# Performance work log

Hardware: AMD Instinct MI355X
Metric: run time of the kernel (lower is better)

The kernel has to match this reference:

```python
import jax, jax.numpy as jnp
import numpy as np

ROPE_THETA = 10000.0

def _apply_rope(x, theta=ROPE_THETA):
    # x: [B, H, L, d_head]
    L, d_k = x.shape[-2], x.shape[-1]
    inv_freq = 1.0 / (theta ** (jnp.arange(0, d_k, 2, dtype=jnp.float32) / d_k))  # [d_k/2]
    ang = jnp.arange(L, dtype=jnp.float32)[:, None] * inv_freq[None, :]           # [L, d_k/2]
    ang = jnp.repeat(ang, 2, axis=-1)                                             # [L, d_k] interleaved
    xr = x.reshape(x.shape[:-1] + (d_k // 2, 2))
    rot = jnp.stack((-xr[..., 1], xr[..., 0]), axis=-1).reshape(x.shape)
    return x * jnp.cos(ang) + rot * jnp.sin(ang)

def setup_inputs() -> dict:
    key = jax.random.key(0)
    k1, k2, k3 = jax.random.split(key, 3)
    B, L, D = 2, 2048, 2048
    std_qkv = np.sqrt(2.0 / (D + 3 * D)).astype(np.float32)
    std_o = np.sqrt(2.0 / (D + D)).astype(np.float32)
    return {
        "x": jax.random.normal(k1, (B, L, D), dtype=jnp.float32),
        "W_qkv": jax.random.normal(k2, (3 * D, D), dtype=jnp.float32) * std_qkv,
        "W_o": jax.random.normal(k3, (D, D), dtype=jnp.float32) * std_o,
    }

def reference(x, W_qkv, W_o):
    B, L, D = x.shape
    H = 16
    dh = D // H
    qkv = jnp.einsum('bld,ed->ble', x, W_qkv)            # [B, L, 3D]
    q, k, v = jnp.split(qkv, 3, axis=-1)
    # [B, H, L, dh]
    q = q.reshape(B, L, H, dh).transpose(0, 2, 1, 3)
    k = k.reshape(B, L, H, dh).transpose(0, 2, 1, 3)
    v = v.reshape(B, L, H, dh).transpose(0, 2, 1, 3)
    q = _apply_rope(q)
    k = _apply_rope(k)
    scale = 1.0 / np.sqrt(dh).astype(np.float32)
    att = jnp.einsum('bhqd,bhkd->bhqk', q, k) * scale    # [B, H, L, L]
    causal = jnp.tril(jnp.ones((L, L), dtype=bool))
    att = jnp.where(causal, att, -jnp.inf)
    p = jax.nn.softmax(att, axis=-1)
    y = jnp.einsum('bhqk,bhkd->bhqd', p, v)              # [B, H, L, dh]
    y = y.transpose(0, 2, 1, 3).reshape(B, L, D)
    return jnp.einsum('bld,ed->ble', y, W_o)
```

## Files before the change

kernel.cpp:

```cpp
#include <hip/hip_runtime.h>
#include <math.h>

typedef __bf16 bf16x8 __attribute__((ext_vector_type(8)));
typedef float f32x4 __attribute__((ext_vector_type(4)));
typedef unsigned short us8 __attribute__((ext_vector_type(8)));

#define B_ 2
#define L_ 2048
#define D_ 2048
#define H_ 16
#define DH 128

__device__ __forceinline__ unsigned short f2b(float f) {
  union { float f; unsigned u; } v; v.f = f;
  unsigned u = v.u;
  return (unsigned short)((u + 0x7fffu + ((u >> 16) & 1u)) >> 16);
}
__device__ __forceinline__ float b2f(unsigned short h) {
  union { unsigned u; float f; } v; v.u = ((unsigned)h) << 16;
  return v.f;
}

#define GLD16(g, l) __builtin_amdgcn_global_load_lds(                          \
    (const __attribute__((address_space(1))) void*)(g),                        \
    (__attribute__((address_space(3))) void*)(l), 16, 0, 0)

#define SBAR() __builtin_amdgcn_s_barrier()
#define LGK0() asm volatile("s_waitcnt lgkmcnt(0)")
#define SCB0() __builtin_amdgcn_sched_barrier(0)
#define VMC6() asm volatile("s_waitcnt vmcnt(6)" ::: "memory")
#define VMC3() asm volatile("s_waitcnt vmcnt(3)" ::: "memory")
#define VMC0() asm volatile("s_waitcnt vmcnt(0)" ::: "memory")

__device__ __forceinline__ unsigned ldsoff(const void* p) {
  return (unsigned)(unsigned long long)(const __attribute__((address_space(3))) char*)p;
}
__device__ __forceinline__ bf16x8 dsr128(unsigned a) {
  bf16x8 r;
  asm volatile("ds_read_b128 %0, %1" : "=v"(r) : "v"(a));
  return r;
}

__global__ void f32_to_bf16_3(const float* __restrict__ a, int na4,
                              const float* __restrict__ b, int nb4,
                              const float* __restrict__ c, int nc4,
                              unsigned short* __restrict__ oa,
                              unsigned short* __restrict__ ob,
                              unsigned short* __restrict__ oc) {
  const int total = na4 + nb4 + nc4;
  int i = blockIdx.x * blockDim.x + threadIdx.x;
  const int stride = gridDim.x * blockDim.x;
  for (; i < total; i += stride) {
    const float* src;
    unsigned short* dst;
    int j = i;
    if (j < na4) { src = a; dst = oa; }
    else if (j < na4 + nb4) { j -= na4; src = b; dst = ob; }
    else { j -= na4 + nb4; src = c; dst = oc; }
    const float4 v = ((const float4*)src)[j];
    ushort4 o;
    o.x = f2b(v.x); o.y = f2b(v.y); o.z = f2b(v.z); o.w = f2b(v.w);
    ((ushort4*)dst)[j] = o;
  }
}

template <bool OUT_BF16>
__global__ __launch_bounds__(256, 2)
void gemmw128(const unsigned short* __restrict__ A,
              const unsigned short* __restrict__ Bm,
              void* __restrict__ Cv, int M, int N, int K) {
  __shared__ __align__(16) unsigned short lA[3][128 * 32];
  __shared__ __align__(16) unsigned short lB[3][256 * 32];
  const int tid = threadIdx.x;
  const int w = tid >> 6, lane = tid & 63;
  const int lo = lane & 15, hi = lane >> 4;
  const int mh = w >> 1;
  const int nh = w & 1;
  const int GM = M >> 7;
  const int nwg = gridDim.x;
  const int f = blockIdx.x;
  const int v = (f & 7) * (nwg >> 3) + (f >> 3);
  const int bn = v / GM, bm = v % GM;
  const int NT = K >> 5;

  const int srow = tid >> 2;
  const int gs = (tid & 3) ^ ((srow >> 1) & 3);
  auto stA = [&](int buf, int u, int tile) {
    GLD16(A + (long)(bm * 128 + u * 64 + srow) * K + tile * 32 + gs * 8,
          &lA[buf][u * 2048 + tid * 8]);
  };
  auto stB = [&](int buf, int u, int tile) {
    GLD16(Bm + (long)(bn * 256 + u * 64 + srow) * K + tile * 32 + gs * 8,
          &lB[buf][u * 2048 + tid * 8]);
  };

  unsigned aoff[4], boff[8];
#pragma unroll
  for (int mi = 0; mi < 4; ++mi) {
    const int r = mh * 64 + mi * 16 + lo;
    aoff[mi] = ldsoff(&lA[0][0]) + r * 64 + ((hi ^ ((r >> 1) & 3)) * 16);
  }
#pragma unroll
  for (int ni = 0; ni < 8; ++ni) {
    const int rb = nh * 128 + ni * 16 + lo;
    boff[ni] = ldsoff(&lB[0][0]) + rb * 64 + ((hi ^ ((rb >> 1) & 3)) * 16);
  }

  f32x4 acc[4][8] = {};

  stA(0, 0, 0); stA(0, 1, 0);
  stB(0, 0, 0); stB(0, 1, 0); stB(0, 2, 0); stB(0, 3, 0);
  stA(1, 0, 1); stA(1, 1, 1);
  stB(1, 0, 1); stB(1, 1, 1); stB(1, 2, 1); stB(1, 3, 1);
  VMC6();
  SBAR();

  for (int t = 0; t < NT; ++t) {
    const int bt = t % 3;
    const int b2 = (t + 2) % 3;
    const bool nx = (t + 2 < NT);
    const unsigned ab = (unsigned)(bt * 8192);
    const unsigned bb = (unsigned)(bt * 16384);
    bf16x8 af[4], bfv[8];
#pragma unroll
    for (int mi = 0; mi < 4; ++mi) af[mi] = dsr128(aoff[mi] + ab);
#pragma unroll
    for (int ni = 0; ni < 8; ++ni) bfv[ni] = dsr128(boff[ni] + bb);
    if (nx) {
      stA(b2, 0, t + 2); stA(b2, 1, t + 2);
      stB(b2, 0, t + 2); stB(b2, 1, t + 2);
      stB(b2, 2, t + 2); stB(b2, 3, t + 2);
    }
    LGK0(); SCB0();
    __builtin_amdgcn_s_setprio(1);
#pragma unroll
    for (int ni = 0; ni < 8; ++ni)
#pragma unroll
      for (int mi = 0; mi < 4; ++mi)
        acc[mi][ni] = __builtin_amdgcn_mfma_f32_16x16x32_bf16(
            af[mi], bfv[ni], acc[mi][ni], 0, 0, 0);
    __builtin_amdgcn_s_setprio(0);
    if (t < NT - 2) VMC6(); else VMC0();
    SBAR();
  }

  const int r0 = bm * 128 + mh * 64;
  const int c0 = bn * 256 + nh * 128;
#pragma unroll
  for (int mi = 0; mi < 4; ++mi) {
#pragma unroll
    for (int r = 0; r < 4; ++r) {
      const long row = r0 + mi * 16 + hi * 4 + r;
#pragma unroll
      for (int ni = 0; ni < 8; ++ni) {
        const int col = c0 + ni * 16 + lo;
        if (OUT_BF16)
          ((unsigned short*)Cv)[row * N + col] = f2b(acc[mi][ni][r]);
        else
          ((float*)Cv)[row * N + col] = acc[mi][ni][r];
      }
    }
  }
}

template <bool OUT_BF16>
__global__ __launch_bounds__(512, 4)
void gemmk32(const unsigned short* __restrict__ A,
             const unsigned short* __restrict__ Bm,
             void* __restrict__ Cv, int M, int N, int K) {
  __shared__ __align__(16) unsigned short lA[3][128 * 32];
  __shared__ __align__(16) unsigned short lB[3][256 * 32];
  const int tid = threadIdx.x;
  const int w = tid >> 6, lane = tid & 63;
  const int lo = lane & 15, hi = lane >> 4;
  const int mh = w >> 2;
  const int wn = (w & 3) * 64;
  const int GM = M >> 7;
  const int nwg = gridDim.x;
  const int f = blockIdx.x;
  const int v = (f & 7) * (nwg >> 3) + (f >> 3);
  const int bn = v / GM, bm = v % GM;
  const int NT = K >> 5;

  const int srow = tid >> 2;
  const int gs = (tid & 3) ^ ((srow >> 1) & 3);
  auto stA = [&](int buf, int tile) {
    GLD16(A + (long)(bm * 128 + srow) * K + tile * 32 + gs * 8,
          &lA[buf][(tid & ~63) * 8]);
  };
  auto stB = [&](int buf, int u, int tile) {
    GLD16(Bm + (long)(bn * 256 + u * 128 + srow) * K + tile * 32 + gs * 8,
          &lB[buf][u * 4096 + (tid & ~63) * 8]);
  };

  unsigned aoff[4], boff[4];
#pragma unroll
  for (int mi = 0; mi < 4; ++mi) {
    const int r = mh * 64 + mi * 16 + lo;
    aoff[mi] = ldsoff(&lA[0][0]) + r * 64 + ((hi ^ ((r >> 1) & 3)) * 16);
  }
#pragma unroll
  for (int ni = 0; ni < 4; ++ni) {
    const int rb = wn + ni * 16 + lo;
    boff[ni] = ldsoff(&lB[0][0]) + rb * 64 + ((hi ^ ((rb >> 1) & 3)) * 16);
  }

  f32x4 acc[4][4] = {};

  stA(0, 0); stB(0, 0, 0); stB(0, 1, 0);
  stA(1, 1); stB(1, 0, 1); stB(1, 1, 1);
  VMC3();
  SBAR();

  for (int t = 0; t < NT; ++t) {
    const int bt = t % 3;
    const int b2 = (t + 2) % 3;
    const bool nx = (t + 2 < NT);
    const unsigned ab = (unsigned)(bt * 8192);
    const unsigned bb = (unsigned)(bt * 16384);
    bf16x8 af[4], bfv[4];
#pragma unroll
    for (int mi = 0; mi < 4; ++mi) af[mi] = dsr128(aoff[mi] + ab);
#pragma unroll
    for (int ni = 0; ni < 4; ++ni) bfv[ni] = dsr128(boff[ni] + bb);
    if (nx) { stA(b2, t + 2); stB(b2, 0, t + 2); stB(b2, 1, t + 2); }
    LGK0(); SCB0();
    __builtin_amdgcn_s_setprio(1);
#pragma unroll
    for (int mi = 0; mi < 4; ++mi)
#pragma unroll
      for (int ni = 0; ni < 4; ++ni)
        acc[mi][ni] = __builtin_amdgcn_mfma_f32_16x16x32_bf16(
            af[mi], bfv[ni], acc[mi][ni], 0, 0, 0);
    __builtin_amdgcn_s_setprio(0);
    if (t < NT - 2) VMC3(); else VMC0();
    SBAR();
  }

  const int r0 = bm * 128 + mh * 64;
  const int c0 = bn * 256 + wn;
#pragma unroll
  for (int mi = 0; mi < 4; ++mi) {
#pragma unroll
    for (int r = 0; r < 4; ++r) {
      const long row = r0 + mi * 16 + hi * 4 + r;
#pragma unroll
      for (int ni = 0; ni < 4; ++ni) {
        const int col = c0 + ni * 16 + lo;
        if (OUT_BF16)
          ((unsigned short*)Cv)[row * N + col] = f2b(acc[mi][ni][r]);
        else
          ((float*)Cv)[row * N + col] = acc[mi][ni][r];
      }
    }
  }
}

__global__ void rope_qk(const unsigned short* __restrict__ qkv,
                        unsigned short* __restrict__ Qo,
                        unsigned short* __restrict__ Ko) {
  const int idx = blockIdx.x * 256 + threadIdx.x;
  const int i = idx & 63;
  const int l = (idx >> 6) & (L_ - 1);
  const int h = (idx >> 17) & (H_ - 1);
  const int b = idx >> 21;
  const float invf = exp2f(-(float)i * 0.20762050593045077f);
  const float ang = (float)l * invf;
  float sn, cs;
  sincosf(ang, &sn, &cs);
  const long base = ((long)b * L_ + l) * (3 * D_) + h * DH + 2 * i;
  const unsigned qin = *(const unsigned*)&qkv[base];
  const unsigned kin = *(const unsigned*)&qkv[base + D_];
  const float q0 = b2f((unsigned short)qin), q1 = b2f((unsigned short)(qin >> 16));
  const float k0 = b2f((unsigned short)kin), k1 = b2f((unsigned short)(kin >> 16));
  const float sc = 0.12751743f;
  const float qo0 = (q0 * cs - q1 * sn) * sc, qo1 = (q1 * cs + q0 * sn) * sc;
  const float ko0 = (k0 * cs - k1 * sn), ko1 = (k1 * cs + k0 * sn);
  const long oo = ((long)(b * H_ + h) * L_ + l) * DH + 2 * i;
  *(unsigned*)&Qo[oo] = (unsigned)f2b(qo0) | ((unsigned)f2b(qo1) << 16);
  *(unsigned*)&Ko[oo] = (unsigned)f2b(ko0) | ((unsigned)f2b(ko1) << 16);
}

__global__ __launch_bounds__(256)
void v_fragpack(const unsigned short* __restrict__ qkv,
                unsigned short* __restrict__ Vf) {
  const int lblk = blockIdx.x;
  const int bh = blockIdx.y;
  const int b = bh >> 4, h = bh & 15;
  __shared__ unsigned short tile[64 * 137];
  const int tid = threadIdx.x;
  const int l0 = lblk * 64;
#pragma unroll
  for (int j = 0; j < 4; ++j) {
    const int c = j * 256 + tid;
    const int row = c >> 4, col8 = c & 15;
    const us8 v = *(const us8*)&qkv[((long)b * L_ + l0 + row) * (3 * D_) +
                                    2 * D_ + h * DH + col8 * 8];
    unsigned short* dst = &tile[row * 137 + col8 * 8];
#pragma unroll
    for (int e = 0; e < 8; ++e) dst[e] = v[e];
  }
  __syncthreads();
#pragma unroll
  for (int j = 0; j < 4; ++j) {
    const int c = j * 256 + tid;
    const int k32l = c >> 9, t2 = (c >> 6) & 7, lane = c & 63;
    const int lo = lane & 15, hi = lane >> 4;
    us8 v;
#pragma unroll
    for (int e = 0; e < 8; ++e)
      v[e] = tile[(k32l * 32 + hi * 8 + e) * 137 + t2 * 16 + lo];
    *(us8*)&Vf[(((size_t)bh * 64 + lblk * 2 + k32l) * 8 + t2) * 512 + lane * 8] = v;
  }
}

__global__ __launch_bounds__(256, 2)
void flash_attn3(const unsigned short* __restrict__ Q,
                 const unsigned short* __restrict__ Kg,
                 const unsigned short* __restrict__ Vf,
                 unsigned short* __restrict__ Y) {
  const int p = blockIdx.x;
  const int tA = p, tB = (L_ / 64 - 1) - p;
  const int h = blockIdx.y, b = blockIdx.z;
  const int tid = threadIdx.x;
  const int wave = tid >> 6, lane = tid & 63;
  const int lo = lane & 15, hi = lane >> 4;
  const int swz = (lo & 7) << 4;
  const int qA = tA * 64 + wave * 16;
  const int qB = tB * 64 + wave * 16;
  const long hoff = ((long)(b * H_ + h)) * L_ * DH;
  const unsigned short* Qh = Q + hoff;
  const unsigned short* Kh = Kg + hoff;
  const unsigned short* Vfh = Vf + ((size_t)(b * H_ + h)) * (64 * 8 * 512);

  __shared__ unsigned short lK[2][64 * 128];
  __shared__ unsigned short pl[4][2][16 * 72];
  unsigned short* plA = &pl[wave][0][0];
  unsigned short* plB = &pl[wave][1][0];

  auto stage = [&](int bufi, int kv0s) {
    unsigned short* bk = &lK[bufi][0];
#pragma unroll
    for (int j = 0; j < 4; ++j) {
      const int c = j * 256 + tid;
      const int row = c >> 4;
      const int soff = ((c & 15) ^ (row & 7)) << 3;
      GLD16(Kh + (long)(kv0s + row) * DH + soff, &bk[(c & ~63) * 8]);
    }
  };

  bf16x8 qfA[4], qfB[4];
#pragma unroll
  for (int s = 0; s < 4; ++s) {
    qfA[s] = *(const bf16x8*)&Qh[(long)(qA + lo) * DH + s * 32 + hi * 8];
    qfB[s] = *(const bf16x8*)&Qh[(long)(qB + lo) * DH + s * 32 + hi * 8];
  }

  float mA = -INFINITY, lsA = 0.f, mB = -INFINITY, lsB = 0.f;
  f32x4 yA[8] = {}, yB[8] = {};

  auto softmax = [&](f32x4 (&st)[4], float& m, float& lsum, f32x4 (&yacc)[8],
                     unsigned short* plw, int qw, int kv0) {
    if (kv0 + 63 > qw) {
      const int d0 = qw + lo - kv0 - hi * 4;
#pragma unroll
      for (int t = 0; t < 4; ++t) {
        const int dt = d0 - t * 16;
#pragma unroll
        for (int r = 0; r < 4; ++r)
          if (r > dt) st[t][r] = -INFINITY;
      }
    }
    float tm0 = fmaxf(fmaxf(st[0][0], st[0][1]), fmaxf(st[0][2], st[0][3]));
    float tm1 = fmaxf(fmaxf(st[1][0], st[1][1]), fmaxf(st[1][2], st[1][3]));
    float tm2 = fmaxf(fmaxf(st[2][0], st[2][1]), fmaxf(st[2][2], st[2][3]));
    float tm3 = fmaxf(fmaxf(st[3][0], st[3][1]), fmaxf(st[3][2], st[3][3]));
    float rm = fmaxf(fmaxf(tm0, tm1), fmaxf(tm2, tm3));
    rm = fmaxf(rm, __shfl_xor(rm, 16));
    rm = fmaxf(rm, __shfl_xor(rm, 32));
    if (!__all(rm <= m + 8.f)) {
      const float mn = fmaxf(m, rm);
      const float alpha = exp2f(m - mn);
      m = mn;
      lsum *= alpha;
      float ar[4];
#pragma unroll
      for (int r = 0; r < 4; ++r) ar[r] = __shfl(alpha, hi * 4 + r);
#pragma unroll
      for (int t2 = 0; t2 < 8; ++t2)
#pragma unroll
        for (int r = 0; r < 4; ++r) yacc[t2][r] *= ar[r];
    }
    float rs = 0.f;
#pragma unroll
    for (int t = 0; t < 4; ++t) {
#pragma unroll
      for (int r2 = 0; r2 < 2; ++r2) {
        const float e0 = exp2f(st[t][2 * r2] - m);
        const float e1 = exp2f(st[t][2 * r2 + 1] - m);
        rs += e0 + e1;
        const unsigned short u0 = __builtin_bit_cast(unsigned short, (__bf16)e0);
        const unsigned short u1 = __builtin_bit_cast(unsigned short, (__bf16)e1);
        *(unsigned*)&plw[lo * 72 + t * 16 + hi * 4 + 2 * r2] =
            (unsigned)u0 | ((unsigned)u1 << 16);
      }
    }
    rs += __shfl_xor(rs, 16);
    rs += __shfl_xor(rs, 32);
    lsum += rs;
  };

  const int nIter = tB + 1;
  stage(0, 0);
  __syncthreads();

  for (int it = 0; it < nIter; ++it) {
    const int kv0 = it * 64;
    const bool aAct = (it <= tA);
    if (it + 1 < nIter) stage((it + 1) & 1, kv0 + 64);
    const char* bkc = (const char*)&lK[it & 1][0];
    f32x4 stA[4] = {}, stB[4] = {};
    if (aAct) {
#pragma unroll
      for (int s = 0; s < 4; ++s) {
        const int inner = (lo * 256 + s * 64 + hi * 16) ^ swz;
#pragma unroll
        for (int t = 0; t < 4; ++t) {
          const bf16x8 kf = *(const bf16x8*)(bkc + t * 4096 + inner);
          stA[t] = __builtin_amdgcn_mfma_f32_16x16x32_bf16(kf, qfA[s], stA[t], 0, 0, 0);
          stB[t] = __builtin_amdgcn_mfma_f32_16x16x32_bf16(kf, qfB[s], stB[t], 0, 0, 0);
        }
      }
    } else {
#pragma unroll
      for (int s = 0; s < 4; ++s) {
        const int inner = (lo * 256 + s * 64 + hi * 16) ^ swz;
#pragma unroll
        for (int t = 0; t < 4; ++t) {
          const bf16x8 kf = *(const bf16x8*)(bkc + t * 4096 + inner);
          stB[t] = __builtin_amdgcn_mfma_f32_16x16x32_bf16(kf, qfB[s], stB[t], 0, 0, 0);
        }
      }
    }
    const unsigned short* vbase = Vfh + (size_t)(it * 16) * 512 + lane * 8;
    bf16x8 vf[16];
#pragma unroll
    for (int t2 = 0; t2 < 16; ++t2)
      vf[t2] = *(const bf16x8*)(vbase + (size_t)t2 * 512);
    if (aAct) softmax(stA, mA, lsA, yA, plA, qA, kv0);
    softmax(stB, mB, lsB, yB, plB, qB, kv0);
#pragma unroll
    for (int kt = 0; kt < 2; ++kt) {
      const bf16x8 pfB = *(const bf16x8*)&plB[lo * 72 + kt * 32 + hi * 8];
#pragma unroll
      for (int t2 = 0; t2 < 8; ++t2)
        yB[t2] = __builtin_amdgcn_mfma_f32_16x16x32_bf16(pfB, vf[kt * 8 + t2], yB[t2], 0, 0, 0);
      if (aAct) {
        const bf16x8 pfA = *(const bf16x8*)&plA[lo * 72 + kt * 32 + hi * 8];
#pragma unroll
        for (int t2 = 0; t2 < 8; ++t2)
          yA[t2] = __builtin_amdgcn_mfma_f32_16x16x32_bf16(pfA, vf[kt * 8 + t2], yA[t2], 0, 0, 0);
      }
    }
    __syncthreads();
  }

  auto wout = [&](f32x4 (&yacc)[8], float lsum, int qw) {
    const float inv = 1.f / lsum;
    float ir[4];
#pragma unroll
    for (int r = 0; r < 4; ++r) ir[r] = __shfl(inv, hi * 4 + r);
#pragma unroll
    for (int r = 0; r < 4; ++r) {
      const long row = qw + hi * 4 + r;
      unsigned short* yrow = Y + ((long)b * L_ + row) * D_ + h * DH;
#pragma unroll
      for (int t2 = 0; t2 < 8; ++t2)
        yrow[t2 * 16 + lo] = f2b(yacc[t2][r] * ir[r]);
    }
  };
  wout(yA, lsA, qA);
  wout(yB, lsB, qB);
}

extern "C" void kernel_launch(void* const* d_in, const int* in_sizes, int n_in,
                              void* d_out, int out_size, void* d_ws, size_t ws_size,
                              hipStream_t stream) {
  const float* x = (const float*)d_in[0];
  const float* wqkv = (const float*)d_in[1];
  const float* wo = (const float*)d_in[2];
  float* out = (float*)d_out;

  unsigned short* ws = (unsigned short*)d_ws;
  const size_t N_X = (size_t)B_ * L_ * D_;
  const size_t N_WQKV = (size_t)3 * D_ * D_;
  const size_t N_WO = (size_t)D_ * D_;
  const size_t N_QKV = (size_t)B_ * L_ * 3 * D_;
  const size_t N_HEAD = (size_t)B_ * H_ * L_ * DH;
  unsigned short* xb = ws;
  unsigned short* wqkb = xb + N_X;
  unsigned short* wob = wqkb + N_WQKV;
  unsigned short* qkv = wob + N_WO;
  unsigned short* Qb = qkv + N_QKV;
  unsigned short* Kb = Qb + N_HEAD;
  unsigned short* Vf = Kb + N_HEAD;
  unsigned short* Yb = Vf + N_HEAD;
  const size_t need = (size_t)(Yb + N_HEAD - ws) * sizeof(unsigned short);
  if (ws_size < need) return;

  f32_to_bf16_3<<<2048, 256, 0, stream>>>(
      x, (int)(N_X / 4), wqkv, (int)(N_WQKV / 4), wo, (int)(N_WO / 4),
      xb, wqkb, wob);

  gemmw128<true><<<(B_ * L_ / 128) * (3 * D_ / 256), 256, 0, stream>>>(
      xb, wqkb, qkv, B_ * L_, 3 * D_, D_);

  rope_qk<<<(B_ * H_ * L_ * 64) / 256, 256, 0, stream>>>(qkv, Qb, Kb);
  v_fragpack<<<dim3(L_ / 64, B_ * H_), 256, 0, stream>>>(qkv, Vf);

  flash_attn3<<<dim3(16, H_, B_), 256, 0, stream>>>(Qb, Kb, Vf, Yb);

  gemmk32<false><<<(B_ * L_ / 128) * (D_ / 256), 512, 0, stream>>>(
      Yb, wob, out, B_ * L_, D_, D_);
}
```

Measured before the change: 278.0 us.

## Fuse RoPE, Q scaling and V fragment packing into QKV GEMM epilogue

The QKV projection GEMM now runs with 512 threads in a 2x4 wave layout, as in the output GEMM. Its epilogue writes Q and K with RoPE and the Q scale applied, and writes V directly in the fragment-packed layout. This removes the separate rope_qk and v_fragpack kernels and the bf16 qkv intermediate round trip through global memory. The cost is heavier epilogue math (hardware sin/cos, shuffles) and scattered 2-byte stores for Q/K, plus the change in wave tiling.

```diff
diff --git a/kernel.cpp b/kernel.cpp
--- a/kernel.cpp
+++ b/kernel.cpp
@@ -28,7 +28,6 @@
 #define SBAR() __builtin_amdgcn_s_barrier()
 #define LGK0() asm volatile("s_waitcnt lgkmcnt(0)")
 #define SCB0() __builtin_amdgcn_sched_barrier(0)
-#define VMC6() asm volatile("s_waitcnt vmcnt(6)" ::: "memory")
 #define VMC3() asm volatile("s_waitcnt vmcnt(3)" ::: "memory")
 #define VMC0() asm volatile("s_waitcnt vmcnt(0)" ::: "memory")
 
@@ -64,18 +63,19 @@
   }
 }
 
-template <bool OUT_BF16>
-__global__ __launch_bounds__(256, 2)
-void gemmw128(const unsigned short* __restrict__ A,
+__global__ __launch_bounds__(512, 4)
+void gemm_qkv(const unsigned short* __restrict__ A,
               const unsigned short* __restrict__ Bm,
-              void* __restrict__ Cv, int M, int N, int K) {
+              unsigned short* __restrict__ Qb,
+              unsigned short* __restrict__ Kb,
+              unsigned short* __restrict__ Vf, int M, int K) {
   __shared__ __align__(16) unsigned short lA[3][128 * 32];
   __shared__ __align__(16) unsigned short lB[3][256 * 32];
   const int tid = threadIdx.x;
   const int w = tid >> 6, lane = tid & 63;
   const int lo = lane & 15, hi = lane >> 4;
-  const int mh = w >> 1;
-  const int nh = w & 1;
+  const int mh = w >> 2;
+  const int wn = (w & 3) * 64;
   const int GM = M >> 7;
   const int nwg = gridDim.x;
   const int f = blockIdx.x;
@@ -85,34 +85,32 @@
 
   const int srow = tid >> 2;
   const int gs = (tid & 3) ^ ((srow >> 1) & 3);
-  auto stA = [&](int buf, int u, int tile) {
-    GLD16(A + (long)(bm * 128 + u * 64 + srow) * K + tile * 32 + gs * 8,
-          &lA[buf][u * 2048 + tid * 8]);
+  auto stA = [&](int buf, int tile) {
+    GLD16(A + (long)(bm * 128 + srow) * K + tile * 32 + gs * 8,
+          &lA[buf][(tid & ~63) * 8]);
   };
   auto stB = [&](int buf, int u, int tile) {
-    GLD16(Bm + (long)(bn * 256 + u * 64 + srow) * K + tile * 32 + gs * 8,
-          &lB[buf][u * 2048 + tid * 8]);
-  };
-
-  unsigned aoff[4], boff[8];
+    GLD16(Bm + (long)(bn * 256 + u * 128 + srow) * K + tile * 32 + gs * 8,
+          &lB[buf][u * 4096 + (tid & ~63) * 8]);
+  };
+
+  unsigned aoff[4], boff[4];
 #pragma unroll
   for (int mi = 0; mi < 4; ++mi) {
     const int r = mh * 64 + mi * 16 + lo;
     aoff[mi] = ldsoff(&lA[0][0]) + r * 64 + ((hi ^ ((r >> 1) & 3)) * 16);
   }
 #pragma unroll
-  for (int ni = 0; ni < 8; ++ni) {
-    const int rb = nh * 128 + ni * 16 + lo;
+  for (int ni = 0; ni < 4; ++ni) {
+    const int rb = wn + ni * 16 + lo;
     boff[ni] = ldsoff(&lB[0][0]) + rb * 64 + ((hi ^ ((rb >> 1) & 3)) * 16);
   }
 
-  f32x4 acc[4][8] = {};
-
-  stA(0, 0, 0); stA(0, 1, 0);
-  stB(0, 0, 0); stB(0, 1, 0); stB(0, 2, 0); stB(0, 3, 0);
-  stA(1, 0, 1); stA(1, 1, 1);
-  stB(1, 0, 1); stB(1, 1, 1); stB(1, 2, 1); stB(1, 3, 1);
-  VMC6();
+  f32x4 acc[4][4] = {};
+
+  stA(0, 0); stB(0, 0, 0); stB(0, 1, 0);
+  stA(1, 1); stB(1, 0, 1); stB(1, 1, 1);
+  VMC3();
   SBAR();
 
   for (int t = 0; t < NT; ++t) {
@@ -121,43 +119,70 @@
     const bool nx = (t + 2 < NT);
     const unsigned ab = (unsigned)(bt * 8192);
     const unsigned bb = (unsigned)(bt * 16384);
-    bf16x8 af[4], bfv[8];
+    bf16x8 af[4], bfv[4];
 #pragma unroll
     for (int mi = 0; mi < 4; ++mi) af[mi] = dsr128(aoff[mi] + ab);
 #pragma unroll
-    for (int ni = 0; ni < 8; ++ni) bfv[ni] = dsr128(boff[ni] + bb);
-    if (nx) {
-      stA(b2, 0, t + 2); stA(b2, 1, t + 2);
-      stB(b2, 0, t + 2); stB(b2, 1, t + 2);
-      stB(b2, 2, t + 2); stB(b2, 3, t + 2);
-    }
+    for (int ni = 0; ni < 4; ++ni) bfv[ni] = dsr128(boff[ni] + bb);
+    if (nx) { stA(b2, t + 2); stB(b2, 0, t + 2); stB(b2, 1, t + 2); }
     LGK0(); SCB0();
     __builtin_amdgcn_s_setprio(1);
 #pragma unroll
-    for (int ni = 0; ni < 8; ++ni)
-#pragma unroll
-      for (int mi = 0; mi < 4; ++mi)
+    for (int mi = 0; mi < 4; ++mi)
+#pragma unroll
+      for (int ni = 0; ni < 4; ++ni)
         acc[mi][ni] = __builtin_amdgcn_mfma_f32_16x16x32_bf16(
             af[mi], bfv[ni], acc[mi][ni], 0, 0, 0);
     __builtin_amdgcn_s_setprio(0);
-    if (t < NT - 2) VMC6(); else VMC0();
+    if (t < NT - 2) VMC3(); else VMC0();
     SBAR();
   }
 
   const int r0 = bm * 128 + mh * 64;
-  const int c0 = bn * 256 + nh * 128;
-#pragma unroll
-  for (int mi = 0; mi < 4; ++mi) {
-#pragma unroll
-    for (int r = 0; r < 4; ++r) {
-      const long row = r0 + mi * 16 + hi * 4 + r;
-#pragma unroll
-      for (int ni = 0; ni < 8; ++ni) {
-        const int col = c0 + ni * 16 + lo;
-        if (OUT_BF16)
-          ((unsigned short*)Cv)[row * N + col] = f2b(acc[mi][ni][r]);
-        else
-          ((float*)Cv)[row * N + col] = acc[mi][ni][r];
+  const int h = (bn & 7) * 2 + (wn >> 7);
+  const int d0 = wn & 64;
+  if (bn < 16) {
+    unsigned short* dst = (bn < 8) ? Qb : Kb;
+    const float sc = (bn < 8) ? 0.12751743f : 1.0f;
+#pragma unroll
+    for (int ni = 0; ni < 4; ++ni) {
+      const int d = d0 + ni * 16 + lo;
+      const float invr = exp2f(-(float)(d >> 1) * 0.20762050593045077f) *
+                         0.15915494309189535f;
+#pragma unroll
+      for (int mi = 0; mi < 4; ++mi) {
+#pragma unroll
+        for (int r = 0; r < 4; ++r) {
+          const int row = r0 + mi * 16 + hi * 4 + r;
+          const int b = row >> 11, l = row & (L_ - 1);
+          const float rev = __builtin_amdgcn_fractf((float)l * invr);
+          const float sn = __builtin_amdgcn_sinf(rev);
+          const float cs = __builtin_amdgcn_cosf(rev);
+          const float v0 = acc[mi][ni][r] * sc;
+          const float vp = __shfl_xor(v0, 1);
+          const float ov = (d & 1) ? (v0 * cs + vp * sn)
+                                   : (v0 * cs - vp * sn);
+          dst[((long)(b * H_ + h) * L_ + l) * DH + d] = f2b(ov);
+        }
+      }
+    }
+  } else {
+#pragma unroll
+    for (int ni = 0; ni < 4; ++ni) {
+      const int d = d0 + ni * 16 + lo;
+#pragma unroll
+      for (int mi = 0; mi < 4; ++mi) {
+        const int row0 = r0 + mi * 16 + hi * 4;
+        const int b = row0 >> 11, l0 = row0 & (L_ - 1);
+        const size_t base =
+            (((size_t)(b * H_ + h) * 64 + (l0 >> 5)) * 8 + (d >> 4)) * 512;
+        const int fl = (d & 15) + ((l0 >> 3) & 3) * 16;
+        ushort4 pk;
+        pk.x = f2b(acc[mi][ni][0]);
+        pk.y = f2b(acc[mi][ni][1]);
+        pk.z = f2b(acc[mi][ni][2]);
+        pk.w = f2b(acc[mi][ni][3]);
+        *(ushort4*)&Vf[base + fl * 8 + (l0 & 7)] = pk;
       }
     }
   }
@@ -256,64 +281,6 @@
   }
 }
 
-__global__ void rope_qk(const unsigned short* __restrict__ qkv,
-                        unsigned short* __restrict__ Qo,
-                        unsigned short* __restrict__ Ko) {
-  const int idx = blockIdx.x * 256 + threadIdx.x;
-  const int i = idx & 63;
-  const int l = (idx >> 6) & (L_ - 1);
-  const int h = (idx >> 17) & (H_ - 1);
-  const int b = idx >> 21;
-  const float invf = exp2f(-(float)i * 0.20762050593045077f);
-  const float ang = (float)l * invf;
-  float sn, cs;
-  sincosf(ang, &sn, &cs);
-  const long base = ((long)b * L_ + l) * (3 * D_) + h * DH + 2 * i;
-  const unsigned qin = *(const unsigned*)&qkv[base];
-  const unsigned kin = *(const unsigned*)&qkv[base + D_];
-  const float q0 = b2f((unsigned short)qin), q1 = b2f((unsigned short)(qin >> 16));
-  const float k0 = b2f((unsigned short)kin), k1 = b2f((unsigned short)(kin >> 16));
-  const float sc = 0.12751743f;
-  const float qo0 = (q0 * cs - q1 * sn) * sc, qo1 = (q1 * cs + q0 * sn) * sc;
-  const float ko0 = (k0 * cs - k1 * sn), ko1 = (k1 * cs + k0 * sn);
-  const long oo = ((long)(b * H_ + h) * L_ + l) * DH + 2 * i;
-  *(unsigned*)&Qo[oo] = (unsigned)f2b(qo0) | ((unsigned)f2b(qo1) << 16);
-  *(unsigned*)&Ko[oo] = (unsigned)f2b(ko0) | ((unsigned)f2b(ko1) << 16);
-}
-
-__global__ __launch_bounds__(256)
-void v_fragpack(const unsigned short* __restrict__ qkv,
-                unsigned short* __restrict__ Vf) {
-  const int lblk = blockIdx.x;
-  const int bh = blockIdx.y;
-  const int b = bh >> 4, h = bh & 15;
-  __shared__ unsigned short tile[64 * 137];
-  const int tid = threadIdx.x;
-  const int l0 = lblk * 64;
-#pragma unroll
-  for (int j = 0; j < 4; ++j) {
-    const int c = j * 256 + tid;
-    const int row = c >> 4, col8 = c & 15;
-    const us8 v = *(const us8*)&qkv[((long)b * L_ + l0 + row) * (3 * D_) +
-                                    2 * D_ + h * DH + col8 * 8];
-    unsigned short* dst = &tile[row * 137 + col8 * 8];
-#pragma unroll
-    for (int e = 0; e < 8; ++e) dst[e] = v[e];
-  }
-  __syncthreads();
-#pragma unroll
-  for (int j = 0; j < 4; ++j) {
-    const int c = j * 256 + tid;
-    const int k32l = c >> 9, t2 = (c >> 6) & 7, lane = c & 63;
-    const int lo = lane & 15, hi = lane >> 4;
-    us8 v;
-#pragma unroll
-    for (int e = 0; e < 8; ++e)
-      v[e] = tile[(k32l * 32 + hi * 8 + e) * 137 + t2 * 16 + lo];
-    *(us8*)&Vf[(((size_t)bh * 64 + lblk * 2 + k32l) * 8 + t2) * 512 + lane * 8] = v;
-  }
-}
-
 __global__ __launch_bounds__(256, 2)
 void flash_attn3(const unsigned short* __restrict__ Q,
                  const unsigned short* __restrict__ Kg,
@@ -495,13 +462,11 @@
   const size_t N_X = (size_t)B_ * L_ * D_;
   const size_t N_WQKV = (size_t)3 * D_ * D_;
   const size_t N_WO = (size_t)D_ * D_;
-  const size_t N_QKV = (size_t)B_ * L_ * 3 * D_;
   const size_t N_HEAD = (size_t)B_ * H_ * L_ * DH;
   unsigned short* xb = ws;
   unsigned short* wqkb = xb + N_X;
   unsigned short* wob = wqkb + N_WQKV;
-  unsigned short* qkv = wob + N_WO;
-  unsigned short* Qb = qkv + N_QKV;
+  unsigned short* Qb = wob + N_WO;
   unsigned short* Kb = Qb + N_HEAD;
   unsigned short* Vf = Kb + N_HEAD;
   unsigned short* Yb = Vf + N_HEAD;
@@ -512,11 +477,8 @@
       x, (int)(N_X / 4), wqkv, (int)(N_WQKV / 4), wo, (int)(N_WO / 4),
       xb, wqkb, wob);
 
-  gemmw128<true><<<(B_ * L_ / 128) * (3 * D_ / 256), 256, 0, stream>>>(
-      xb, wqkb, qkv, B_ * L_, 3 * D_, D_);
-
-  rope_qk<<<(B_ * H_ * L_ * 64) / 256, 256, 0, stream>>>(qkv, Qb, Kb);
-  v_fragpack<<<dim3(L_ / 64, B_ * H_), 256, 0, stream>>>(qkv, Vf);
+  gemm_qkv<<<(B_ * L_ / 128) * (3 * D_ / 256), 512, 0, stream>>>(
+      xb, wqkb, Qb, Kb, Vf, B_ * L_, D_);
 
   flash_attn3<<<dim3(16, H_, B_), 256, 0, stream>>>(Qb, Kb, Vf, Yb);
 
```

Result: faster. 259.8 us (-6.5%).
